# Kernel tuning notes

Measured on AMD Instinct MI355X. Metric: run time of the kernel, lower is better.

## Reference

```python
import jax, jax.numpy as jnp
import numpy as np

N_NODES = 200000
N_EDGES = 600000


def gcn_conv(x, src, dst, W, b, n):
    # PyG GCNConv: linear (no bias), add self-loops, symmetric degree norm,
    # scatter-add aggregation, then bias.
    h = x @ W                                   # [N, out]
    loop = jnp.arange(n, dtype=src.dtype)
    src_f = jnp.concatenate([src, loop])        # [E+N]
    dst_f = jnp.concatenate([dst, loop])
    deg = jax.ops.segment_sum(jnp.ones_like(dst_f, dtype=h.dtype), dst_f,
                              num_segments=n)   # in-degree incl. self loops
    dinv = jnp.where(deg > 0, jax.lax.rsqrt(deg), 0.0)
    norm = dinv[src_f] * dinv[dst_f]            # [E+N]
    msg = h[src_f] * norm[:, None]              # gather + scale
    out = jax.ops.segment_sum(msg, dst_f, num_segments=n)
    return out + b


def setup_inputs() -> dict:
    key = jax.random.key(0)
    ks = jax.random.split(key, 8)
    x = jax.random.normal(ks[0], (N_NODES, 2), dtype=jnp.float32)
    edge_index = jax.random.randint(ks[1], (2, N_EDGES), 0, N_NODES, dtype=jnp.int64)
    def glorot(k, fan_in, fan_out):
        s = jnp.sqrt(6.0 / (fan_in + fan_out))
        return jax.random.uniform(k, (fan_in, fan_out), jnp.float32, -s, s)
    return {
        "x": x,
        "edge_index": edge_index,
        "W1": glorot(ks[2], 2, 128),
        "b1": jnp.zeros((128,), jnp.float32),
        "W2": glorot(ks[3], 128, 64),
        "b2": jnp.zeros((64,), jnp.float32),
        "Wp": glorot(ks[4], 64, 1),
        "bp": jnp.zeros((1,), jnp.float32),
    }


def reference(x, edge_index, W1, b1, W2, b2, Wp, bp):
    src, dst = edge_index[0], edge_index[1]
    n = x.shape[0]
    h = jax.nn.relu(gcn_conv(x, src, dst, W1, b1, n))
    h = jax.nn.relu(gcn_conv(h, src, dst, W2, b2, n))
    return jax.nn.sigmoid(h @ Wp + bp).squeeze(-1)   # [N]
```

## Files before the change

### kernel.cpp

```cpp
#include <hip/hip_runtime.h>
#include <hip/hip_fp16.h>
#include <math.h>

typedef _Float16 f16x8 __attribute__((ext_vector_type(8)));
typedef float f32x4 __attribute__((ext_vector_type(4)));

constexpr int SCAN_TPB = 256;
constexpr int SCAN_EPT = 8;
constexpr int SCAN_EPB = SCAN_TPB * SCAN_EPT;

__global__ __launch_bounds__(256) void k_init(const float* __restrict__ W2,
                                              __half* __restrict__ w2t,
                                              int* __restrict__ deg, int n) {
    int idx = blockIdx.x * 256 + threadIdx.x;
    if (idx < 128 * 64) {
        int k = idx >> 6, f = idx & 63;
        w2t[f * 128 + k] = __float2half(W2[idx]);
    }
    int n4 = n >> 2;
    int4* d4 = reinterpret_cast<int4*>(deg);
    int stride = gridDim.x * 256;
    for (int j = idx; j < n4; j += stride) d4[j] = make_int4(0, 0, 0, 0);
    for (int j = (n4 << 2) + idx; j < n; j += stride) deg[j] = 0;
}

__global__ void k_deg(const int* __restrict__ dst, int* __restrict__ deg, int E) {
    int i = blockIdx.x * blockDim.x + threadIdx.x;
    if (i < E) atomicAdd(&deg[dst[i]], 1);
}

__global__ __launch_bounds__(SCAN_TPB) void k_blocksum(const int* __restrict__ deg,
                                                       int* __restrict__ bsum, int n) {
    int t = threadIdx.x;
    int idx0 = blockIdx.x * SCAN_EPB + t * SCAN_EPT;
    int s = 0;
    if (idx0 + SCAN_EPT <= n) {
        const int4* p = reinterpret_cast<const int4*>(deg + idx0);
        int4 a = p[0], b = p[1];
        s = a.x + a.y + a.z + a.w + b.x + b.y + b.z + b.w;
    } else {
        for (int k = 0; k < SCAN_EPT; ++k) { int i = idx0 + k; if (i < n) s += deg[i]; }
    }
#pragma unroll
    for (int off = 32; off; off >>= 1) s += __shfl_xor(s, off);
    __shared__ int wsum[4];
    int lane = t & 63, wid = t >> 6;
    if (lane == 0) wsum[wid] = s;
    __syncthreads();
    if (t == 0) bsum[blockIdx.x] = wsum[0] + wsum[1] + wsum[2] + wsum[3];
}

__global__ __launch_bounds__(SCAN_TPB) void k_scanfinal(const int* __restrict__ deg,
                                                        const int* __restrict__ bsum,
                                                        int nb,
                                                        int* __restrict__ row_off,
                                                        int* __restrict__ cursor,
                                                        const float2* __restrict__ x2,
                                                        float* __restrict__ dinv,
                                                        float2* __restrict__ xsc, int n) {
    int t = threadIdx.x, lane = t & 63, wid = t >> 6;
    __shared__ int wsumA[4], wsumB[4], wsumC[4];
    __shared__ int s_add;
    int bid = blockIdx.x;
    int partial = 0;
    for (int j = t; j < bid; j += SCAN_TPB) partial += bsum[j];
#pragma unroll
    for (int off = 32; off; off >>= 1) partial += __shfl_xor(partial, off);
    if (lane == 0) wsumA[wid] = partial;
    if (bid == (int)gridDim.x - 1) {
        int tot = 0;
        for (int j = t; j < nb; j += SCAN_TPB) tot += bsum[j];
#pragma unroll
        for (int off = 32; off; off >>= 1) tot += __shfl_xor(tot, off);
        if (lane == 0) wsumB[wid] = tot;
    }
    __syncthreads();
    if (t == 0) {
        s_add = wsumA[0] + wsumA[1] + wsumA[2] + wsumA[3];
        if (bid == (int)gridDim.x - 1)
            row_off[n] = wsumB[0] + wsumB[1] + wsumB[2] + wsumB[3];
    }

    int idx0 = bid * SCAN_EPB + t * SCAN_EPT;
    int e[SCAN_EPT];
    bool full = (idx0 + SCAN_EPT <= n);
    if (full) {
        const int4* p = reinterpret_cast<const int4*>(deg + idx0);
        int4 a = p[0], b = p[1];
        e[0] = a.x; e[1] = a.y; e[2] = a.z; e[3] = a.w;
        e[4] = b.x; e[5] = b.y; e[6] = b.z; e[7] = b.w;
    } else {
        for (int k = 0; k < SCAN_EPT; ++k) { int i = idx0 + k; e[k] = (i < n) ? deg[i] : 0; }
    }
#pragma unroll
    for (int k = 0; k < SCAN_EPT; ++k) {
        int i = idx0 + k;
        if (i < n) {
            float di = rsqrtf((float)e[k] + 1.0f);
            dinv[i] = di;
            float2 xv = x2[i];
            xsc[i] = make_float2(xv.x * di, xv.y * di);
        }
    }
    int tsum = 0;
#pragma unroll
    for (int k = 0; k < SCAN_EPT; ++k) tsum += e[k];
    int s = tsum;
#pragma unroll
    for (int off = 1; off < 64; off <<= 1) { int u = __shfl_up(s, off); if (lane >= off) s += u; }
    if (lane == 63) wsumC[wid] = s;
    __syncthreads();
    int add = s_add;
    for (int w = 0; w < wid; ++w) add += wsumC[w];
    int run = s - tsum + add;
    int o[SCAN_EPT];
#pragma unroll
    for (int k = 0; k < SCAN_EPT; ++k) { o[k] = run; run += e[k]; }
    if (full) {
        int4* ro = reinterpret_cast<int4*>(row_off + idx0);
        int4* cu = reinterpret_cast<int4*>(cursor + idx0);
        ro[0] = make_int4(o[0], o[1], o[2], o[3]);
        ro[1] = make_int4(o[4], o[5], o[6], o[7]);
        cu[0] = make_int4(o[0], o[1], o[2], o[3]);
        cu[1] = make_int4(o[4], o[5], o[6], o[7]);
    } else {
        for (int k = 0; k < SCAN_EPT; ++k) {
            int i = idx0 + k;
            if (i < n) { row_off[i] = o[k]; cursor[i] = o[k]; }
        }
    }
}

__global__ void k_fill(const int* __restrict__ src, const int* __restrict__ dst,
                       int* __restrict__ cursor, int* __restrict__ csr_src, int E) {
    int e = blockIdx.x * blockDim.x + threadIdx.x;
    if (e < E) {
        int pos = atomicAdd(&cursor[dst[e]], 1);
        csr_src[pos] = src[e];
    }
}

__global__ __launch_bounds__(256) void k_agg1(
    const float2* __restrict__ xsc, const float* __restrict__ dinv,
    const int* __restrict__ row_off, const int* __restrict__ csr_src,
    float2* __restrict__ xam, int n) {
    int i = blockIdx.x * blockDim.x + threadIdx.x;
    if (i >= n) return;
    int r0 = row_off[i], r1 = row_off[i + 1];
    float2 self = xsc[i];
    float xa0 = self.x, xa1 = self.y;
    for (int j = r0; j < r1; ++j) {
        float2 v = xsc[csr_src[j]];
        xa0 += v.x; xa1 += v.y;
    }
    float di = dinv[i];
    xam[i] = make_float2(xa0 * di, xa1 * di);
}

__global__ __launch_bounds__(256, 2) void k_gemm1m(
    const float2* __restrict__ xam, const float* __restrict__ W1,
    const float* __restrict__ b1, const __half* __restrict__ w2t,
    const float* __restrict__ dinv, __half* __restrict__ m2h, int n) {
    __shared__ __align__(16) float cs[4][16][68];
    int tid = threadIdx.x;
    int w = tid >> 6, lane = tid & 63;
    int col = lane & 15, kg = lane >> 4;
    int base = (blockIdx.x * 4 + w) * 16;

    f16x8 bf[4][4];
#pragma unroll
    for (int ft = 0; ft < 4; ++ft)
#pragma unroll
        for (int t = 0; t < 4; ++t)
            bf[ft][t] = *reinterpret_cast<const f16x8*>(
                w2t + (ft * 16 + col) * 128 + t * 32 + kg * 8);

    int an = base + col; if (an >= n) an = 0;
    float2 xa = xam[an];
    f32x4 c0 = {}, c1 = {}, c2 = {}, c3 = {};
#pragma unroll
    for (int t = 0; t < 4; ++t) {
        int k0 = t * 32 + kg * 8;
        float4 wa0 = *reinterpret_cast<const float4*>(&W1[k0]);
        float4 wa1 = *reinterpret_cast<const float4*>(&W1[k0 + 4]);
        float4 wb0 = *reinterpret_cast<const float4*>(&W1[128 + k0]);
        float4 wb1 = *reinterpret_cast<const float4*>(&W1[128 + k0 + 4]);
        float4 bb0 = *reinterpret_cast<const float4*>(&b1[k0]);
        float4 bb1 = *reinterpret_cast<const float4*>(&b1[k0 + 4]);
        f16x8 a;
        a[0] = (_Float16)fmaxf(fmaf(xa.y, wb0.x, fmaf(xa.x, wa0.x, bb0.x)), 0.f);
        a[1] = (_Float16)fmaxf(fmaf(xa.y, wb0.y, fmaf(xa.x, wa0.y, bb0.y)), 0.f);
        a[2] = (_Float16)fmaxf(fmaf(xa.y, wb0.z, fmaf(xa.x, wa0.z, bb0.z)), 0.f);
        a[3] = (_Float16)fmaxf(fmaf(xa.y, wb0.w, fmaf(xa.x, wa0.w, bb0.w)), 0.f);
        a[4] = (_Float16)fmaxf(fmaf(xa.y, wb1.x, fmaf(xa.x, wa1.x, bb1.x)), 0.f);
        a[5] = (_Float16)fmaxf(fmaf(xa.y, wb1.y, fmaf(xa.x, wa1.y, bb1.y)), 0.f);
        a[6] = (_Float16)fmaxf(fmaf(xa.y, wb1.z, fmaf(xa.x, wa1.z, bb1.z)), 0.f);
        a[7] = (_Float16)fmaxf(fmaf(xa.y, wb1.w, fmaf(xa.x, wa1.w, bb1.w)), 0.f);
        c0 = __builtin_amdgcn_mfma_f32_16x16x32_f16(a, bf[0][t], c0, 0, 0, 0);
        c1 = __builtin_amdgcn_mfma_f32_16x16x32_f16(a, bf[1][t], c1, 0, 0, 0);
        c2 = __builtin_amdgcn_mfma_f32_16x16x32_f16(a, bf[2][t], c2, 0, 0, 0);
        c3 = __builtin_amdgcn_mfma_f32_16x16x32_f16(a, bf[3][t], c3, 0, 0, 0);
    }
#pragma unroll
    for (int r = 0; r < 4; ++r) {
        cs[w][kg * 4 + r][0 * 16 + col] = c0[r];
        cs[w][kg * 4 + r][1 * 16 + col] = c1[r];
        cs[w][kg * 4 + r][2 * 16 + col] = c2[r];
        cs[w][kg * 4 + r][3 * 16 + col] = c3[r];
    }
    __syncthreads();
    int nl = tid >> 2, ch = tid & 3;
    int node = blockIdx.x * 64 + nl;
    if (node < n) {
        float di = dinv[node];
        const float* row = &cs[nl >> 4][nl & 15][ch * 16];
        union { __half2 h2v[8]; int4 q[2]; } u;
#pragma unroll
        for (int j = 0; j < 8; ++j)
            u.h2v[j] = __floats2half2_rn(row[2 * j] * di, row[2 * j + 1] * di);
        int4* dst = reinterpret_cast<int4*>(m2h + (size_t)node * 64 + ch * 16);
        dst[0] = u.q[0]; dst[1] = u.q[1];
    }
}

__global__ __launch_bounds__(256) void k_l2out(
    const __half* __restrict__ m2h, const float* __restrict__ dinv,
    const int* __restrict__ row_off, const int* __restrict__ csr_src,
    const float* __restrict__ b2, const float* __restrict__ Wp,
    const float* __restrict__ bp, float* __restrict__ out, int n) {
    int tid = threadIdx.x;
    int wid = tid >> 6, lane = tid & 63;
    int g = lane >> 3;
    int f8 = lane & 7;
    int i = (blockIdx.x * 4 + wid) * 8 + g;
    bool valid = i < n;
    int ic = valid ? i : 0;
    int r0 = row_off[ic];
    int r1 = valid ? row_off[ic + 1] : r0;
    int4 sv = *reinterpret_cast<const int4*>(m2h + (size_t)ic * 64 + f8 * 8);
    const __half2* sh = reinterpret_cast<const __half2*>(&sv);
    __half2 a0 = sh[0], a1 = sh[1], a2 = sh[2], a3 = sh[3];
    __half2 z; z.x = __ushort_as_half((unsigned short)0); z.y = z.x;
    __half2 b0 = z, b1 = z, b2v_ = z, b3 = z;
    int j = r0;
    for (; j + 1 < r1; j += 2) {
        int s0 = csr_src[j], s1 = csr_src[j + 1];
        int4 v0 = *reinterpret_cast<const int4*>(m2h + (size_t)s0 * 64 + f8 * 8);
        int4 v1 = *reinterpret_cast<const int4*>(m2h + (size_t)s1 * 64 + f8 * 8);
        const __half2* h0 = reinterpret_cast<const __half2*>(&v0);
        const __half2* h1 = reinterpret_cast<const __half2*>(&v1);
        a0 = __hadd2(a0, h0[0]); a1 = __hadd2(a1, h0[1]);
        a2 = __hadd2(a2, h0[2]); a3 = __hadd2(a3, h0[3]);
        b0 = __hadd2(b0, h1[0]); b1 = __hadd2(b1, h1[1]);
        b2v_ = __hadd2(b2v_, h1[2]); b3 = __hadd2(b3, h1[3]);
    }
    if (j < r1) {
        int s0 = csr_src[j];
        int4 v0 = *reinterpret_cast<const int4*>(m2h + (size_t)s0 * 64 + f8 * 8);
        const __half2* h0 = reinterpret_cast<const __half2*>(&v0);
        a0 = __hadd2(a0, h0[0]); a1 = __hadd2(a1, h0[1]);
        a2 = __hadd2(a2, h0[2]); a3 = __hadd2(a3, h0[3]);
    }
    a0 = __hadd2(a0, b0); a1 = __hadd2(a1, b1);
    a2 = __hadd2(a2, b2v_); a3 = __hadd2(a3, b3);
    float2 f0 = __half22float2(a0), f1 = __half22float2(a1);
    float2 f2 = __half22float2(a2), f3 = __half22float2(a3);
    float di = dinv[ic];
    float4 b2a = reinterpret_cast<const float4*>(b2)[f8 * 2];
    float4 b2b = reinterpret_cast<const float4*>(b2)[f8 * 2 + 1];
    float4 wpa = reinterpret_cast<const float4*>(Wp)[f8 * 2];
    float4 wpb = reinterpret_cast<const float4*>(Wp)[f8 * 2 + 1];
    float v = fmaxf(fmaf(f0.x, di, b2a.x), 0.f) * wpa.x
            + fmaxf(fmaf(f0.y, di, b2a.y), 0.f) * wpa.y
            + fmaxf(fmaf(f1.x, di, b2a.z), 0.f) * wpa.z
            + fmaxf(fmaf(f1.y, di, b2a.w), 0.f) * wpa.w
            + fmaxf(fmaf(f2.x, di, b2b.x), 0.f) * wpb.x
            + fmaxf(fmaf(f2.y, di, b2b.y), 0.f) * wpb.y
            + fmaxf(fmaf(f3.x, di, b2b.z), 0.f) * wpb.z
            + fmaxf(fmaf(f3.y, di, b2b.w), 0.f) * wpb.w;
    v += __shfl_xor(v, 1);
    v += __shfl_xor(v, 2);
    v += __shfl_xor(v, 4);
    if (valid && f8 == 0) out[i] = 1.f / (1.f + expf(-(v + bp[0])));
}

extern "C" void kernel_launch(void* const* d_in, const int* in_sizes, int n_in,
                              void* d_out, int out_size, void* d_ws, size_t ws_size,
                              hipStream_t stream) {
    const float* x  = (const float*)d_in[0];
    const int*   ei = (const int*)d_in[1];
    const float* W1 = (const float*)d_in[2];
    const float* b1 = (const float*)d_in[3];
    const float* W2 = (const float*)d_in[4];
    const float* b2 = (const float*)d_in[5];
    const float* Wp = (const float*)d_in[6];
    const float* bp = (const float*)d_in[7];
    float* out = (float*)d_out;

    int n = in_sizes[0] / 2;
    int E = in_sizes[1] / 2;
    const int* src = ei;
    const int* dst = ei + E;

    char* ws = (char*)d_ws;
    size_t off = 0;
    auto alloc = [&](size_t bytes) -> void* {
        void* p = ws + off;
        off += (bytes + 255) & ~(size_t)255;
        return p;
    };
    int nb = (n + SCAN_EPB - 1) / SCAN_EPB;
    int*    deg     = (int*)alloc((size_t)n * 4);
    int*    bsum    = (int*)alloc((size_t)nb * 4);
    int*    row_off = (int*)alloc((size_t)(n + 1) * 4);
    int*    cursor  = (int*)alloc((size_t)n * 4);
    float*  dinv    = (float*)alloc((size_t)n * 4);
    float2* xsc     = (float2*)alloc((size_t)n * 8);
    float2* xam     = (float2*)alloc((size_t)n * 8);
    int*    csr_src = (int*)alloc((size_t)E * 4);
    __half* w2t     = (__half*)alloc((size_t)128 * 64 * 2);
    __half* m2h     = (__half*)alloc((size_t)n * 64 * 2);
    (void)ws_size;

    k_init     <<<256, 256, 0, stream>>>(W2, w2t, deg, n);
    k_deg      <<<(E + 255) / 256, 256, 0, stream>>>(dst, deg, E);
    k_blocksum <<<nb, SCAN_TPB, 0, stream>>>(deg, bsum, n);
    k_scanfinal<<<nb, SCAN_TPB, 0, stream>>>(deg, bsum, nb, row_off, cursor,
                                             (const float2*)x, dinv, xsc, n);
    k_fill     <<<(E + 255) / 256, 256, 0, stream>>>(src, dst, cursor, csr_src, E);
    k_agg1     <<<(n + 255) / 256, 256, 0, stream>>>(xsc, dinv, row_off, csr_src, xam, n);
    k_gemm1m   <<<(n + 63) / 64, 256, 0, stream>>>(xam, W1, b1, w2t, dinv, m2h, n);
    k_l2out    <<<(n + 31) / 32, 256, 0, stream>>>(m2h, dinv, row_off, csr_src,
                                                   b2, Wp, bp, out, n);
}
```

Measured before the change: 141.0 us.

## Use single-pass decoupled scan and fuse layer-1 aggregation into CSR fill via atomics

Replaces the two-kernel block-sum plus scan with one scan kernel in which each block publishes its aggregate to a flag slot and spin-waits on the slots of earlier blocks. The layer-1 CSR aggregation kernel is removed: the edge fill kernel now also atomically adds scaled source features into a zeroed accumulator, and the self term and normalization are applied in the GEMM kernel. The layer-2 gather loop is unrolled to four edges per iteration for more memory-level parallelism. Together these cut two kernel launches, in exchange for float atomics that make the summation order nondeterministic and a spin-wait that relies on earlier blocks being scheduled first.

```diff
diff --git a/kernel.cpp b/kernel.cpp
--- a/kernel.cpp
+++ b/kernel.cpp
@@ -11,17 +11,24 @@
 
 __global__ __launch_bounds__(256) void k_init(const float* __restrict__ W2,
                                               __half* __restrict__ w2t,
-                                              int* __restrict__ deg, int n) {
+                                              int* __restrict__ deg,
+                                              float* __restrict__ xamacc,
+                                              int* __restrict__ slots, int nb, int n) {
     int idx = blockIdx.x * 256 + threadIdx.x;
     if (idx < 128 * 64) {
         int k = idx >> 6, f = idx & 63;
         w2t[f * 128 + k] = __float2half(W2[idx]);
     }
+    if (idx < nb) slots[idx] = 0;
+    int stride = gridDim.x * 256;
     int n4 = n >> 2;
     int4* d4 = reinterpret_cast<int4*>(deg);
-    int stride = gridDim.x * 256;
     for (int j = idx; j < n4; j += stride) d4[j] = make_int4(0, 0, 0, 0);
     for (int j = (n4 << 2) + idx; j < n; j += stride) deg[j] = 0;
+    int m4 = (2 * n) >> 2;
+    float4* x4 = reinterpret_cast<float4*>(xamacc);
+    for (int j = idx; j < m4; j += stride) x4[j] = make_float4(0.f, 0.f, 0.f, 0.f);
+    for (int j = (m4 << 2) + idx; j < 2 * n; j += stride) xamacc[j] = 0.f;
 }
 
 __global__ void k_deg(const int* __restrict__ dst, int* __restrict__ deg, int E) {
@@ -29,57 +36,17 @@
     if (i < E) atomicAdd(&deg[dst[i]], 1);
 }
 
-__global__ __launch_bounds__(SCAN_TPB) void k_blocksum(const int* __restrict__ deg,
-                                                       int* __restrict__ bsum, int n) {
-    int t = threadIdx.x;
-    int idx0 = blockIdx.x * SCAN_EPB + t * SCAN_EPT;
-    int s = 0;
-    if (idx0 + SCAN_EPT <= n) {
-        const int4* p = reinterpret_cast<const int4*>(deg + idx0);
-        int4 a = p[0], b = p[1];
-        s = a.x + a.y + a.z + a.w + b.x + b.y + b.z + b.w;
-    } else {
-        for (int k = 0; k < SCAN_EPT; ++k) { int i = idx0 + k; if (i < n) s += deg[i]; }
-    }
-#pragma unroll
-    for (int off = 32; off; off >>= 1) s += __shfl_xor(s, off);
-    __shared__ int wsum[4];
-    int lane = t & 63, wid = t >> 6;
-    if (lane == 0) wsum[wid] = s;
-    __syncthreads();
-    if (t == 0) bsum[blockIdx.x] = wsum[0] + wsum[1] + wsum[2] + wsum[3];
-}
-
-__global__ __launch_bounds__(SCAN_TPB) void k_scanfinal(const int* __restrict__ deg,
-                                                        const int* __restrict__ bsum,
-                                                        int nb,
-                                                        int* __restrict__ row_off,
-                                                        int* __restrict__ cursor,
-                                                        const float2* __restrict__ x2,
-                                                        float* __restrict__ dinv,
-                                                        float2* __restrict__ xsc, int n) {
+__global__ __launch_bounds__(SCAN_TPB) void k_scan(const int* __restrict__ deg,
+                                                   int* __restrict__ slots, int nb,
+                                                   int* __restrict__ row_off,
+                                                   int* __restrict__ cursor,
+                                                   const float2* __restrict__ x2,
+                                                   float* __restrict__ dinv,
+                                                   float2* __restrict__ xsc, int n) {
     int t = threadIdx.x, lane = t & 63, wid = t >> 6;
-    __shared__ int wsumA[4], wsumB[4], wsumC[4];
-    __shared__ int s_add;
     int bid = blockIdx.x;
-    int partial = 0;
-    for (int j = t; j < bid; j += SCAN_TPB) partial += bsum[j];
-#pragma unroll
-    for (int off = 32; off; off >>= 1) partial += __shfl_xor(partial, off);
-    if (lane == 0) wsumA[wid] = partial;
-    if (bid == (int)gridDim.x - 1) {
-        int tot = 0;
-        for (int j = t; j < nb; j += SCAN_TPB) tot += bsum[j];
-#pragma unroll
-        for (int off = 32; off; off >>= 1) tot += __shfl_xor(tot, off);
-        if (lane == 0) wsumB[wid] = tot;
-    }
-    __syncthreads();
-    if (t == 0) {
-        s_add = wsumA[0] + wsumA[1] + wsumA[2] + wsumA[3];
-        if (bid == (int)gridDim.x - 1)
-            row_off[n] = wsumB[0] + wsumB[1] + wsumB[2] + wsumB[3];
-    }
+    __shared__ int wsum[4], wscan[4];
+    __shared__ int s_add, s_agg;
 
     int idx0 = bid * SCAN_EPB + t * SCAN_EPT;
     int e[SCAN_EPT];
@@ -105,13 +72,40 @@
     int tsum = 0;
 #pragma unroll
     for (int k = 0; k < SCAN_EPT; ++k) tsum += e[k];
+    int r = tsum;
+#pragma unroll
+    for (int off = 32; off; off >>= 1) r += __shfl_xor(r, off);
+    if (lane == 0) wsum[wid] = r;
+    __syncthreads();
+    if (t == 0) {
+        int agg = wsum[0] + wsum[1] + wsum[2] + wsum[3];
+        s_agg = agg;
+        atomicExch(&slots[bid], (agg << 1) | 1);
+    }
+    if (wid == 0) {
+        int acc = 0;
+        for (int base = 0; base < bid; base += 64) {
+            int j = base + lane;
+            if (j < bid) {
+                int v;
+                do { v = atomicAdd(&slots[j], 0); } while (!(v & 1));
+                acc += v >> 1;
+            }
+        }
+#pragma unroll
+        for (int off = 32; off; off >>= 1) acc += __shfl_xor(acc, off);
+        if (lane == 0) s_add = acc;
+    }
+    __syncthreads();
+    if (t == 0 && bid == (int)gridDim.x - 1) row_off[n] = s_add + s_agg;
+
     int s = tsum;
 #pragma unroll
     for (int off = 1; off < 64; off <<= 1) { int u = __shfl_up(s, off); if (lane >= off) s += u; }
-    if (lane == 63) wsumC[wid] = s;
+    if (lane == 63) wscan[wid] = s;
     __syncthreads();
     int add = s_add;
-    for (int w = 0; w < wid; ++w) add += wsumC[w];
+    for (int w = 0; w < wid; ++w) add += wscan[w];
     int run = s - tsum + add;
     int o[SCAN_EPT];
 #pragma unroll
@@ -131,36 +125,26 @@
     }
 }
 
-__global__ void k_fill(const int* __restrict__ src, const int* __restrict__ dst,
-                       int* __restrict__ cursor, int* __restrict__ csr_src, int E) {
+__global__ void k_fillagg(const int* __restrict__ src, const int* __restrict__ dst,
+                          const float2* __restrict__ xsc,
+                          int* __restrict__ cursor, int* __restrict__ csr_src,
+                          float* __restrict__ xamacc, int E) {
     int e = blockIdx.x * blockDim.x + threadIdx.x;
     if (e < E) {
-        int pos = atomicAdd(&cursor[dst[e]], 1);
-        csr_src[pos] = src[e];
-    }
-}
-
-__global__ __launch_bounds__(256) void k_agg1(
-    const float2* __restrict__ xsc, const float* __restrict__ dinv,
-    const int* __restrict__ row_off, const int* __restrict__ csr_src,
-    float2* __restrict__ xam, int n) {
-    int i = blockIdx.x * blockDim.x + threadIdx.x;
-    if (i >= n) return;
-    int r0 = row_off[i], r1 = row_off[i + 1];
-    float2 self = xsc[i];
-    float xa0 = self.x, xa1 = self.y;
-    for (int j = r0; j < r1; ++j) {
-        float2 v = xsc[csr_src[j]];
-        xa0 += v.x; xa1 += v.y;
-    }
-    float di = dinv[i];
-    xam[i] = make_float2(xa0 * di, xa1 * di);
+        int d = dst[e], s = src[e];
+        int pos = atomicAdd(&cursor[d], 1);
+        csr_src[pos] = s;
+        float2 v = xsc[s];
+        atomicAdd(&xamacc[2 * d], v.x);
+        atomicAdd(&xamacc[2 * d + 1], v.y);
+    }
 }
 
 __global__ __launch_bounds__(256, 2) void k_gemm1m(
-    const float2* __restrict__ xam, const float* __restrict__ W1,
-    const float* __restrict__ b1, const __half* __restrict__ w2t,
-    const float* __restrict__ dinv, __half* __restrict__ m2h, int n) {
+    const float* __restrict__ xamacc, const float2* __restrict__ xsc,
+    const float* __restrict__ W1, const float* __restrict__ b1,
+    const __half* __restrict__ w2t, const float* __restrict__ dinv,
+    __half* __restrict__ m2h, int n) {
     __shared__ __align__(16) float cs[4][16][68];
     int tid = threadIdx.x;
     int w = tid >> 6, lane = tid & 63;
@@ -176,7 +160,10 @@
                 w2t + (ft * 16 + col) * 128 + t * 32 + kg * 8);
 
     int an = base + col; if (an >= n) an = 0;
-    float2 xa = xam[an];
+    float2 self = xsc[an];
+    float diA = dinv[an];
+    float2 xa = make_float2((xamacc[2 * an] + self.x) * diA,
+                            (xamacc[2 * an + 1] + self.y) * diA);
     f32x4 c0 = {}, c1 = {}, c2 = {}, c3 = {};
 #pragma unroll
     for (int t = 0; t < 4; ++t) {
@@ -242,24 +229,37 @@
     __half2 a0 = sh[0], a1 = sh[1], a2 = sh[2], a3 = sh[3];
     __half2 z; z.x = __ushort_as_half((unsigned short)0); z.y = z.x;
     __half2 b0 = z, b1 = z, b2v_ = z, b3 = z;
-    int j = r0;
-    for (; j + 1 < r1; j += 2) {
-        int s0 = csr_src[j], s1 = csr_src[j + 1];
-        int4 v0 = *reinterpret_cast<const int4*>(m2h + (size_t)s0 * 64 + f8 * 8);
-        int4 v1 = *reinterpret_cast<const int4*>(m2h + (size_t)s1 * 64 + f8 * 8);
-        const __half2* h0 = reinterpret_cast<const __half2*>(&v0);
-        const __half2* h1 = reinterpret_cast<const __half2*>(&v1);
-        a0 = __hadd2(a0, h0[0]); a1 = __hadd2(a1, h0[1]);
-        a2 = __hadd2(a2, h0[2]); a3 = __hadd2(a3, h0[3]);
-        b0 = __hadd2(b0, h1[0]); b1 = __hadd2(b1, h1[1]);
-        b2v_ = __hadd2(b2v_, h1[2]); b3 = __hadd2(b3, h1[3]);
-    }
-    if (j < r1) {
+    for (int j = r0; j < r1; j += 4) {
+        bool d0 = true, d1 = j + 1 < r1, d2 = j + 2 < r1, d3 = j + 3 < r1;
         int s0 = csr_src[j];
-        int4 v0 = *reinterpret_cast<const int4*>(m2h + (size_t)s0 * 64 + f8 * 8);
-        const __half2* h0 = reinterpret_cast<const __half2*>(&v0);
-        a0 = __hadd2(a0, h0[0]); a1 = __hadd2(a1, h0[1]);
-        a2 = __hadd2(a2, h0[2]); a3 = __hadd2(a3, h0[3]);
+        int s1 = d1 ? csr_src[j + 1] : 0;
+        int s2 = d2 ? csr_src[j + 2] : 0;
+        int s3 = d3 ? csr_src[j + 3] : 0;
+        int4 v0, v1, v2, v3;
+        v0 = *reinterpret_cast<const int4*>(m2h + (size_t)s0 * 64 + f8 * 8);
+        if (d1) v1 = *reinterpret_cast<const int4*>(m2h + (size_t)s1 * 64 + f8 * 8);
+        if (d2) v2 = *reinterpret_cast<const int4*>(m2h + (size_t)s2 * 64 + f8 * 8);
+        if (d3) v3 = *reinterpret_cast<const int4*>(m2h + (size_t)s3 * 64 + f8 * 8);
+        {
+            const __half2* h0 = reinterpret_cast<const __half2*>(&v0);
+            a0 = __hadd2(a0, h0[0]); a1 = __hadd2(a1, h0[1]);
+            a2 = __hadd2(a2, h0[2]); a3 = __hadd2(a3, h0[3]);
+        }
+        if (d1) {
+            const __half2* h1 = reinterpret_cast<const __half2*>(&v1);
+            b0 = __hadd2(b0, h1[0]); b1 = __hadd2(b1, h1[1]);
+            b2v_ = __hadd2(b2v_, h1[2]); b3 = __hadd2(b3, h1[3]);
+        }
+        if (d2) {
+            const __half2* h2 = reinterpret_cast<const __half2*>(&v2);
+            a0 = __hadd2(a0, h2[0]); a1 = __hadd2(a1, h2[1]);
+            a2 = __hadd2(a2, h2[2]); a3 = __hadd2(a3, h2[3]);
+        }
+        if (d3) {
+            const __half2* h3 = reinterpret_cast<const __half2*>(&v3);
+            b0 = __hadd2(b0, h3[0]); b1 = __hadd2(b1, h3[1]);
+            b2v_ = __hadd2(b2v_, h3[2]); b3 = __hadd2(b3, h3[3]);
+        }
     }
     a0 = __hadd2(a0, b0); a1 = __hadd2(a1, b1);
     a2 = __hadd2(a2, b2v_); a3 = __hadd2(a3, b3);
@@ -311,25 +311,24 @@
     };
     int nb = (n + SCAN_EPB - 1) / SCAN_EPB;
     int*    deg     = (int*)alloc((size_t)n * 4);
-    int*    bsum    = (int*)alloc((size_t)nb * 4);
+    int*    slots   = (int*)alloc((size_t)nb * 4);
     int*    row_off = (int*)alloc((size_t)(n + 1) * 4);
     int*    cursor  = (int*)alloc((size_t)n * 4);
     float*  dinv    = (float*)alloc((size_t)n * 4);
     float2* xsc     = (float2*)alloc((size_t)n * 8);
-    float2* xam     = (float2*)alloc((size_t)n * 8);
+    float*  xamacc  = (float*)alloc((size_t)n * 8);
     int*    csr_src = (int*)alloc((size_t)E * 4);
     __half* w2t     = (__half*)alloc((size_t)128 * 64 * 2);
     __half* m2h     = (__half*)alloc((size_t)n * 64 * 2);
     (void)ws_size;
 
-    k_init     <<<256, 256, 0, stream>>>(W2, w2t, deg, n);
-    k_deg      <<<(E + 255) / 256, 256, 0, stream>>>(dst, deg, E);
-    k_blocksum <<<nb, SCAN_TPB, 0, stream>>>(deg, bsum, n);
-    k_scanfinal<<<nb, SCAN_TPB, 0, stream>>>(deg, bsum, nb, row_off, cursor,
-                                             (const float2*)x, dinv, xsc, n);
-    k_fill     <<<(E + 255) / 256, 256, 0, stream>>>(src, dst, cursor, csr_src, E);
-    k_agg1     <<<(n + 255) / 256, 256, 0, stream>>>(xsc, dinv, row_off, csr_src, xam, n);
-    k_gemm1m   <<<(n + 63) / 64, 256, 0, stream>>>(xam, W1, b1, w2t, dinv, m2h, n);
-    k_l2out    <<<(n + 31) / 32, 256, 0, stream>>>(m2h, dinv, row_off, csr_src,
-                                                   b2, Wp, bp, out, n);
-}
+    k_init   <<<256, 256, 0, stream>>>(W2, w2t, deg, xamacc, slots, nb, n);
+    k_deg    <<<(E + 255) / 256, 256, 0, stream>>>(dst, deg, E);
+    k_scan   <<<nb, SCAN_TPB, 0, stream>>>(deg, slots, nb, row_off, cursor,
+                                           (const float2*)x, dinv, xsc, n);
+    k_fillagg<<<(E + 255) / 256, 256, 0, stream>>>(src, dst, xsc, cursor, csr_src,
+                                                   xamacc, E);
+    k_gemm1m <<<(n + 63) / 64, 256, 0, stream>>>(xamacc, xsc, W1, b1, w2t, dinv, m2h, n);
+    k_l2out  <<<(n + 31) / 32, 256, 0, stream>>>(m2h, dinv, row_off, csr_src,
+                                                 b2, Wp, bp, out, n);
+}
```

Measured after the change: 190.2 us. 1.35x slower.
